# Optimization experiments

Hardware: AMD Instinct MI355X
Metric: run time of the kernel (lower is better)

The kernel has to match this reference:

```python
import jax, jax.numpy as jnp
import numpy as np

HIDDEN_DIM = 64  # self.hidden_dim = inc
N = 16384
C = 64


def setup_inputs() -> dict:
    key = jax.random.key(0)
    k1, k2, k3, k4, k5 = jax.random.split(key, 5)
    scale = 1.0 / np.sqrt(C)
    return {
        "hidden": jax.random.normal(k1, (N, C), dtype=jnp.float32),
        "query": jax.random.normal(k2, (N, C), dtype=jnp.float32),
        "Wq": jax.random.normal(k3, (C, C), dtype=jnp.float32) * scale,
        "Wk": jax.random.normal(k4, (C, C), dtype=jnp.float32) * scale,
        "Wv": jax.random.normal(k5, (C, C), dtype=jnp.float32) * scale,
    }


def reference(hidden, query, Wq, Wk, Wv):
    # Per-voxel linear projections (center-tap of the sparse 3x3x3 convs)
    q = query @ Wq            # [Nq, C]
    k = hidden @ Wk           # [Nk, C]
    v = hidden @ Wv           # [Nk, C]
    # score = q @ k.T / sqrt(hidden_dim)
    score = jnp.einsum("qc,kc->qk", q, k) / jnp.sqrt(jnp.float32(HIDDEN_DIM))
    attn = jax.nn.softmax(score, axis=-1)  # [Nq, Nk]
    weight = attn @ v         # [Nq, C] -> new hidden.F
    return weight
```

## Files before the change

### kernel.cpp

```cpp
#include <hip/hip_runtime.h>
#include <hip/hip_bf16.h>

#define NT 16384
#define CD 64

typedef __attribute__((ext_vector_type(8))) short bf16x8;
typedef __attribute__((ext_vector_type(16))) float f32x16;
typedef __attribute__((ext_vector_type(2))) int int2v;

#define AS1 __attribute__((address_space(1)))
#define AS3 __attribute__((address_space(3)))

__global__ __launch_bounds__(256) void proj_kernel(
    const float* __restrict__ hidden, const float* __restrict__ query,
    const float* __restrict__ Wq, const float* __restrict__ Wk, const float* __restrict__ Wv,
    __hip_bfloat16* __restrict__ qb, __hip_bfloat16* __restrict__ kb,
    __hip_bfloat16* __restrict__ vTb)
{
    __shared__ float qin[32][64];
    __shared__ float hin[32][64];
    const int tid = threadIdx.x;
    const int R0 = blockIdx.x * 32;
    {
        int r = tid >> 3, c0 = (tid & 7) * 8;
        const float4* qs = (const float4*)(query + (size_t)(R0 + r) * CD + c0);
        const float4* hs = (const float4*)(hidden + (size_t)(R0 + r) * CD + c0);
        *(float4*)&qin[r][c0]     = qs[0];
        *(float4*)&qin[r][c0 + 4] = qs[1];
        *(float4*)&hin[r][c0]     = hs[0];
        *(float4*)&hin[r][c0 + 4] = hs[1];
    }
    __syncthreads();
    const int c = tid & 63, rg = tid >> 6;
    const float SC = 0.18033688011112042f;
    float aq[8] = {0.f}, ak[8] = {0.f}, av[8] = {0.f};
    #pragma unroll 4
    for (int j = 0; j < 64; ++j) {
        float wq = Wq[j * 64 + c], wk = Wk[j * 64 + c], wv = Wv[j * 64 + c];
        #pragma unroll
        for (int r8 = 0; r8 < 8; ++r8) {
            float qv = qin[rg * 8 + r8][j];
            float hv = hin[rg * 8 + r8][j];
            aq[r8] += qv * wq;
            ak[r8] += hv * wk;
            av[r8] += hv * wv;
        }
    }
    #pragma unroll
    for (int r8 = 0; r8 < 8; ++r8) {
        int row = R0 + rg * 8 + r8;
        qb[(size_t)row * CD + c] = __float2bfloat16(aq[r8] * SC);
        kb[(size_t)row * CD + c] = __float2bfloat16(ak[r8]);
    }
    union { bf16x8 v; __hip_bfloat16 h[8]; } u;
    #pragma unroll
    for (int r8 = 0; r8 < 8; ++r8) u.h[r8] = __float2bfloat16(av[r8]);
    *(bf16x8*)(vTb + (size_t)c * NT + R0 + rg * 8) = u.v;
}

__device__ __forceinline__ void stage_tiles(
    char* kdst, char* vdst,
    const __hip_bfloat16* kb, const __hip_bfloat16* vTb,
    int kv, int wid, int lane)
{
    const char* kt = (const char*)(kb + (size_t)kv * CD);
    #pragma unroll
    for (int j = 0; j < 2; ++j) {
        int ob = (wid * 2 + j) * 1024;
        int o  = ob + lane * 16;
        int so = o ^ (((o >> 7) & 7) << 4);
        __builtin_amdgcn_global_load_lds((const AS1 void*)(kt + so),
                                         (AS3 void*)(kdst + ob), 16, 0, 0);
    }
    #pragma unroll
    for (int j = 0; j < 2; ++j) {
        int ob = (wid * 2 + j) * 1024;
        int o  = ob + lane * 16;
        int c  = o >> 7;
        int colb = (o & 127) ^ ((c & 7) << 4);
        __builtin_amdgcn_global_load_lds(
            (const AS1 void*)((const char*)vTb + ((size_t)c * NT + kv) * 2 + colb),
            (AS3 void*)(vdst + ob), 16, 0, 0);
    }
}

__global__ __launch_bounds__(256, 3) void flash_kernel(
    const __hip_bfloat16* __restrict__ qb, const __hip_bfloat16* __restrict__ kb,
    const __hip_bfloat16* __restrict__ vTb,
    float* __restrict__ part, float* __restrict__ lbuf, float* __restrict__ out,
    int nsplit, int kvlen)
{
    __shared__ __align__(16) char kbuf[2][8192];
    __shared__ __align__(16) char vbuf[2][8192];
    __shared__ float llds[4][32];

    const int tid  = threadIdx.x;
    const int lane = tid & 63, wid = tid >> 6;
    const int l31 = lane & 31, h = lane >> 5;
    const int split = blockIdx.x % nsplit;
    const int qblk  = blockIdx.x / nsplit;
    const int q0  = qblk * 128 + wid * 32;
    const int kv0 = split * kvlen;
    const int ntile = kvlen / 64;

    bf16x8 Qf[4];
    #pragma unroll
    for (int cc = 0; cc < 4; ++cc)
        Qf[cc] = *(const bf16x8*)(qb + (size_t)(q0 + l31) * CD + cc * 16 + h * 8);

    f32x16 acc[2];
    #pragma unroll
    for (int dt = 0; dt < 2; ++dt)
        #pragma unroll
        for (int r = 0; r < 16; ++r) acc[dt][r] = 0.f;
    float lsum = 0.f;

    const int krow0 = l31,  krow1 = 32 + l31;
    const int kswz  = (l31 & 7) << 4;

    stage_tiles(kbuf[0], vbuf[0], kb, vTb, kv0, wid, lane);
    asm volatile("s_waitcnt vmcnt(0)" ::: "memory");
    __syncthreads();

    for (int t = 0; t < ntile; ++t) {
        const int b = t & 1;
        if (t + 1 < ntile)
            stage_tiles(kbuf[b ^ 1], vbuf[b ^ 1], kb, vTb, kv0 + (t + 1) * 64, wid, lane);

        f32x16 s0, s1;
        #pragma unroll
        for (int r = 0; r < 16; ++r) { s0[r] = 0.f; s1[r] = 0.f; }
        #pragma unroll
        for (int cc = 0; cc < 4; ++cc) {
            int colb = cc * 32 + h * 16;
            bf16x8 k0 = *(const bf16x8*)(kbuf[b] + krow0 * 128 + (colb ^ kswz));
            bf16x8 k1 = *(const bf16x8*)(kbuf[b] + krow1 * 128 + (colb ^ kswz));
            s0 = __builtin_amdgcn_mfma_f32_32x32x16_bf16(k0, Qf[cc], s0, 0, 0, 0);
            s1 = __builtin_amdgcn_mfma_f32_32x32x16_bf16(k1, Qf[cc], s1, 0, 0, 0);
        }

        float p0[16], p1[16];
        #pragma unroll
        for (int r = 0; r < 16; ++r) {
            p0[r] = __builtin_amdgcn_exp2f(s0[r]);
            p1[r] = __builtin_amdgcn_exp2f(s1[r]);
        }
        {
            float tsub[4];
            #pragma unroll
            for (int j = 0; j < 4; ++j)
                tsub[j] = ((p0[4*j] + p0[4*j+1]) + (p0[4*j+2] + p0[4*j+3]))
                        + ((p1[4*j] + p1[4*j+1]) + (p1[4*j+2] + p1[4*j+3]));
            lsum += (tsub[0] + tsub[1]) + (tsub[2] + tsub[3]);
        }

        int w0[8], w1[8];
        #pragma unroll
        for (int r2 = 0; r2 < 4; ++r2)
            #pragma unroll
            for (int u = 0; u < 2; ++u) {
                asm("v_cvt_pk_bf16_f32 %0, %1, %2"
                    : "=v"(w0[r2 * 2 + u]) : "v"(p0[4*r2 + 2*u]), "v"(p0[4*r2 + 2*u + 1]));
                asm("v_cvt_pk_bf16_f32 %0, %1, %2"
                    : "=v"(w1[r2 * 2 + u]) : "v"(p1[4*r2 + 2*u]), "v"(p1[4*r2 + 2*u + 1]));
            }

        int paw[4][4];
        #pragma unroll
        for (int r2e = 0; r2e < 4; r2e += 2)
            #pragma unroll
            for (int u = 0; u < 2; ++u) {
                int2v ra = __builtin_amdgcn_permlane32_swap(w0[r2e*2 + u], w0[(r2e+1)*2 + u], false, false);
                int kc0 = (r2e >> 1);
                paw[kc0][u] = ra.x; paw[kc0][2 + u] = ra.y;
                int2v rb = __builtin_amdgcn_permlane32_swap(w1[r2e*2 + u], w1[(r2e+1)*2 + u], false, false);
                int kc1 = 2 + (r2e >> 1);
                paw[kc1][u] = rb.x; paw[kc1][2 + u] = rb.y;
            }

        #pragma unroll
        for (int kc = 0; kc < 4; ++kc) {
            union { int i[4]; bf16x8 v; } pu;
            #pragma unroll
            for (int j = 0; j < 4; ++j) pu.i[j] = paw[kc][j];
            #pragma unroll
            for (int dt = 0; dt < 2; ++dt) {
                int row = dt * 32 + l31;
                int colb = kc * 32 + h * 16;
                bf16x8 vf = *(const bf16x8*)(vbuf[b] + row * 128 + (colb ^ kswz));
                acc[dt] = __builtin_amdgcn_mfma_f32_32x32x16_bf16(pu.v, vf, acc[dt], 0, 0, 0);
            }
        }

        asm volatile("s_waitcnt vmcnt(0)" ::: "memory");
        __syncthreads();
    }

    float lfull = lsum + __shfl_xor(lsum, 32);

    if (nsplit == 1) {
        llds[wid][l31] = lfull;
        __builtin_amdgcn_wave_barrier();
        float rl[8];
        #pragma unroll
        for (int rr = 0; rr < 8; ++rr) {
            int qrow = (rr & 3) + 8 * (rr >> 2) + 4 * h;
            rl[rr] = 1.f / llds[wid][qrow];
        }
        #pragma unroll
        for (int dt = 0; dt < 2; ++dt)
            #pragma unroll
            for (int r = 0; r < 16; ++r) {
                int rr = (r & 3) + 4 * (r >> 2);
                (void)rr;
            }
        #pragma unroll
        for (int dt = 0; dt < 2; ++dt)
            #pragma unroll
            for (int r = 0; r < 16; ++r) {
                int qrow = (r & 3) + 8 * (r >> 2) + 4 * h;
                out[(size_t)(q0 + qrow) * CD + dt * 32 + l31] = acc[dt][r] * rl[(r & 3) + 4 * (r >> 2)];
            }
    } else {
        float* pb = part + ((size_t)split * NT + q0) * CD;
        #pragma unroll
        for (int dt = 0; dt < 2; ++dt)
            #pragma unroll
            for (int r = 0; r < 16; ++r) {
                int qrow = (r & 3) + 8 * (r >> 2) + 4 * h;
                pb[qrow * CD + dt * 32 + l31] = acc[dt][r];
            }
        if (h == 0)
            lbuf[(size_t)split * NT + q0 + l31] = lfull;
    }
}

__global__ __launch_bounds__(256) void combine_kernel(
    const float* __restrict__ part, const float* __restrict__ lbuf,
    float* __restrict__ out, int S)
{
    const int tid = threadIdx.x;
    const int row = blockIdx.x * 4 + (tid >> 6);
    const int c = tid & 63;
    float L = 0.f, o = 0.f;
    for (int s = 0; s < S; ++s) {
        L += lbuf[(size_t)s * NT + row];
        o += part[((size_t)s * NT + row) * CD + c];
    }
    out[(size_t)row * CD + c] = o / L;
}

extern "C" void kernel_launch(void* const* d_in, const int* in_sizes, int n_in,
                              void* d_out, int out_size, void* d_ws, size_t ws_size,
                              hipStream_t stream)
{
    (void)in_sizes; (void)n_in; (void)out_size;
    const float* hidden = (const float*)d_in[0];
    const float* query  = (const float*)d_in[1];
    const float* Wq = (const float*)d_in[2];
    const float* Wk = (const float*)d_in[3];
    const float* Wv = (const float*)d_in[4];
    float* out = (float*)d_out;

    char* ws = (char*)d_ws;
    __hip_bfloat16* qb  = (__hip_bfloat16*)ws;
    __hip_bfloat16* kb  = qb + (size_t)NT * CD;
    __hip_bfloat16* vTb = kb + (size_t)NT * CD;
    const size_t base = (size_t)3 * NT * CD * 2;
    const size_t per  = (size_t)NT * CD * 4 + (size_t)NT * 4;

    int S = 1;
    if (ws_size >= base + 8 * per) S = 8;
    else if (ws_size >= base + 4 * per) S = 4;
    else if (ws_size >= base + 2 * per) S = 2;

    float* part = (float*)(ws + base);
    float* lbuf = (float*)(ws + base + (size_t)S * NT * CD * 4);

    hipLaunchKernelGGL(proj_kernel, dim3(NT / 32), dim3(256), 0, stream,
                       hidden, query, Wq, Wk, Wv, qb, kb, vTb);
    hipLaunchKernelGGL(flash_kernel, dim3((NT / 128) * S), dim3(256), 0, stream,
                       qb, kb, vTb, part, lbuf, out, S, NT / S);
    if (S > 1)
        hipLaunchKernelGGL(combine_kernel, dim3(NT / 4), dim3(256), 0, stream,
                           part, lbuf, out, S);
}
```

Before: 104.9 us.

## Load V directly from global, bf16 partials, more splits, setprio around MFMA

V fragments are now loaded straight from global memory into registers each tile rather than staged through LDS, which halves LDS use and permits four blocks per CU. The split-K partial outputs are stored as bf16, halving the workspace traffic in the combine step, and up to 16 splits are allowed. s_setprio is raised around the MFMA sections, and the normalisation divides per element instead of using precomputed reciprocals. The costs are uncoalesced per-lane global V loads with latency exposed inside the loop, and reduced precision in the partial sums.

Result: slower. 225.8 us (+115.4%).

```diff
diff --git a/kernel.cpp b/kernel.cpp
--- a/kernel.cpp
+++ b/kernel.cpp
@@ -58,10 +58,8 @@
     *(bf16x8*)(vTb + (size_t)c * NT + R0 + rg * 8) = u.v;
 }
 
-__device__ __forceinline__ void stage_tiles(
-    char* kdst, char* vdst,
-    const __hip_bfloat16* kb, const __hip_bfloat16* vTb,
-    int kv, int wid, int lane)
+__device__ __forceinline__ void stage_k(
+    char* kdst, const __hip_bfloat16* kb, int kv, int wid, int lane)
 {
     const char* kt = (const char*)(kb + (size_t)kv * CD);
     #pragma unroll
@@ -72,26 +70,15 @@
         __builtin_amdgcn_global_load_lds((const AS1 void*)(kt + so),
                                          (AS3 void*)(kdst + ob), 16, 0, 0);
     }
-    #pragma unroll
-    for (int j = 0; j < 2; ++j) {
-        int ob = (wid * 2 + j) * 1024;
-        int o  = ob + lane * 16;
-        int c  = o >> 7;
-        int colb = (o & 127) ^ ((c & 7) << 4);
-        __builtin_amdgcn_global_load_lds(
-            (const AS1 void*)((const char*)vTb + ((size_t)c * NT + kv) * 2 + colb),
-            (AS3 void*)(vdst + ob), 16, 0, 0);
-    }
-}
-
-__global__ __launch_bounds__(256, 3) void flash_kernel(
+}
+
+__global__ __launch_bounds__(256, 4) void flash_kernel(
     const __hip_bfloat16* __restrict__ qb, const __hip_bfloat16* __restrict__ kb,
     const __hip_bfloat16* __restrict__ vTb,
-    float* __restrict__ part, float* __restrict__ lbuf, float* __restrict__ out,
+    __hip_bfloat16* __restrict__ part, float* __restrict__ lbuf, float* __restrict__ out,
     int nsplit, int kvlen)
 {
     __shared__ __align__(16) char kbuf[2][8192];
-    __shared__ __align__(16) char vbuf[2][8192];
     __shared__ float llds[4][32];
 
     const int tid  = threadIdx.x;
@@ -115,21 +102,25 @@
         for (int r = 0; r < 16; ++r) acc[dt][r] = 0.f;
     float lsum = 0.f;
 
-    const int krow0 = l31,  krow1 = 32 + l31;
+    const int krow0 = l31, krow1 = 32 + l31;
     const int kswz  = (l31 & 7) << 4;
-
-    stage_tiles(kbuf[0], vbuf[0], kb, vTb, kv0, wid, lane);
+    const __hip_bfloat16* vrow0 = vTb + (size_t)(l31) * NT + h * 8;
+    const __hip_bfloat16* vrow1 = vTb + (size_t)(32 + l31) * NT + h * 8;
+
+    stage_k(kbuf[0], kb, kv0, wid, lane);
     asm volatile("s_waitcnt vmcnt(0)" ::: "memory");
     __syncthreads();
 
     for (int t = 0; t < ntile; ++t) {
         const int b = t & 1;
+        const int kv = kv0 + t * 64;
         if (t + 1 < ntile)
-            stage_tiles(kbuf[b ^ 1], vbuf[b ^ 1], kb, vTb, kv0 + (t + 1) * 64, wid, lane);
+            stage_k(kbuf[b ^ 1], kb, kv + 64, wid, lane);
 
         f32x16 s0, s1;
         #pragma unroll
         for (int r = 0; r < 16; ++r) { s0[r] = 0.f; s1[r] = 0.f; }
+        __builtin_amdgcn_s_setprio(1);
         #pragma unroll
         for (int cc = 0; cc < 4; ++cc) {
             int colb = cc * 32 + h * 16;
@@ -137,6 +128,14 @@
             bf16x8 k1 = *(const bf16x8*)(kbuf[b] + krow1 * 128 + (colb ^ kswz));
             s0 = __builtin_amdgcn_mfma_f32_32x32x16_bf16(k0, Qf[cc], s0, 0, 0, 0);
             s1 = __builtin_amdgcn_mfma_f32_32x32x16_bf16(k1, Qf[cc], s1, 0, 0, 0);
+        }
+        __builtin_amdgcn_s_setprio(0);
+
+        bf16x8 Vg[2][4];
+        #pragma unroll
+        for (int kc = 0; kc < 4; ++kc) {
+            Vg[0][kc] = *(const bf16x8*)(vrow0 + kv + kc * 16);
+            Vg[1][kc] = *(const bf16x8*)(vrow1 + kv + kc * 16);
         }
 
         float p0[16], p1[16];
@@ -178,19 +177,16 @@
                 paw[kc1][u] = rb.x; paw[kc1][2 + u] = rb.y;
             }
 
+        __builtin_amdgcn_s_setprio(1);
         #pragma unroll
         for (int kc = 0; kc < 4; ++kc) {
             union { int i[4]; bf16x8 v; } pu;
             #pragma unroll
             for (int j = 0; j < 4; ++j) pu.i[j] = paw[kc][j];
-            #pragma unroll
-            for (int dt = 0; dt < 2; ++dt) {
-                int row = dt * 32 + l31;
-                int colb = kc * 32 + h * 16;
-                bf16x8 vf = *(const bf16x8*)(vbuf[b] + row * 128 + (colb ^ kswz));
-                acc[dt] = __builtin_amdgcn_mfma_f32_32x32x16_bf16(pu.v, vf, acc[dt], 0, 0, 0);
-            }
-        }
+            acc[0] = __builtin_amdgcn_mfma_f32_32x32x16_bf16(pu.v, Vg[0][kc], acc[0], 0, 0, 0);
+            acc[1] = __builtin_amdgcn_mfma_f32_32x32x16_bf16(pu.v, Vg[1][kc], acc[1], 0, 0, 0);
+        }
+        __builtin_amdgcn_s_setprio(0);
 
         asm volatile("s_waitcnt vmcnt(0)" ::: "memory");
         __syncthreads();
@@ -201,34 +197,21 @@
     if (nsplit == 1) {
         llds[wid][l31] = lfull;
         __builtin_amdgcn_wave_barrier();
-        float rl[8];
-        #pragma unroll
-        for (int rr = 0; rr < 8; ++rr) {
-            int qrow = (rr & 3) + 8 * (rr >> 2) + 4 * h;
-            rl[rr] = 1.f / llds[wid][qrow];
-        }
-        #pragma unroll
-        for (int dt = 0; dt < 2; ++dt)
-            #pragma unroll
-            for (int r = 0; r < 16; ++r) {
-                int rr = (r & 3) + 4 * (r >> 2);
-                (void)rr;
-            }
         #pragma unroll
         for (int dt = 0; dt < 2; ++dt)
             #pragma unroll
             for (int r = 0; r < 16; ++r) {
                 int qrow = (r & 3) + 8 * (r >> 2) + 4 * h;
-                out[(size_t)(q0 + qrow) * CD + dt * 32 + l31] = acc[dt][r] * rl[(r & 3) + 4 * (r >> 2)];
+                out[(size_t)(q0 + qrow) * CD + dt * 32 + l31] = acc[dt][r] / llds[wid][qrow];
             }
     } else {
-        float* pb = part + ((size_t)split * NT + q0) * CD;
+        __hip_bfloat16* pb = part + ((size_t)split * NT + q0) * CD;
         #pragma unroll
         for (int dt = 0; dt < 2; ++dt)
             #pragma unroll
             for (int r = 0; r < 16; ++r) {
                 int qrow = (r & 3) + 8 * (r >> 2) + 4 * h;
-                pb[qrow * CD + dt * 32 + l31] = acc[dt][r];
+                pb[qrow * CD + dt * 32 + l31] = __float2bfloat16(acc[dt][r]);
             }
         if (h == 0)
             lbuf[(size_t)split * NT + q0 + l31] = lfull;
@@ -236,7 +219,7 @@
 }
 
 __global__ __launch_bounds__(256) void combine_kernel(
-    const float* __restrict__ part, const float* __restrict__ lbuf,
+    const __hip_bfloat16* __restrict__ part, const float* __restrict__ lbuf,
     float* __restrict__ out, int S)
 {
     const int tid = threadIdx.x;
@@ -245,7 +228,7 @@
     float L = 0.f, o = 0.f;
     for (int s = 0; s < S; ++s) {
         L += lbuf[(size_t)s * NT + row];
-        o += part[((size_t)s * NT + row) * CD + c];
+        o += __bfloat162float(part[((size_t)s * NT + row) * CD + c]);
     }
     out[(size_t)row * CD + c] = o / L;
 }
@@ -267,15 +250,16 @@
     __hip_bfloat16* kb  = qb + (size_t)NT * CD;
     __hip_bfloat16* vTb = kb + (size_t)NT * CD;
     const size_t base = (size_t)3 * NT * CD * 2;
-    const size_t per  = (size_t)NT * CD * 4 + (size_t)NT * 4;
+    const size_t per  = (size_t)NT * CD * 2 + (size_t)NT * 4;
 
     int S = 1;
-    if (ws_size >= base + 8 * per) S = 8;
+    if (ws_size >= base + 16 * per) S = 16;
+    else if (ws_size >= base + 8 * per) S = 8;
     else if (ws_size >= base + 4 * per) S = 4;
     else if (ws_size >= base + 2 * per) S = 2;
 
-    float* part = (float*)(ws + base);
-    float* lbuf = (float*)(ws + base + (size_t)S * NT * CD * 4);
+    __hip_bfloat16* part = (__hip_bfloat16*)(ws + base);
+    float* lbuf = (float*)(ws + base + (size_t)S * NT * CD * 2);
 
     hipLaunchKernelGGL(proj_kernel, dim3(NT / 32), dim3(256), 0, stream,
                        hidden, query, Wq, Wk, Wv, qb, kb, vTb);
```
